# Kernel tuning notes

Hardware: AMD Instinct MI355X
Metric: run time of the kernel (lower is better)

## Reference

```python
import jax, jax.numpy as jnp
import numpy as np

NUM_ENT, NUM_REL, ES = 100000, 200, 128
B, N, K = 4, 1024, 50  # batch of tasks, triples per task, max one-hop neighbors


def setup_inputs() -> dict:
    key = jax.random.key(0)
    ks = jax.random.split(key, 10)
    return {
        "ent_emb": jax.random.normal(ks[0], (NUM_ENT, ES), jnp.float32),
        "rel_emb": jax.random.normal(ks[1], (NUM_REL, ES), jnp.float32),
        "W_bil": jax.random.normal(ks[2], (ES, ES), jnp.float32) * 0.05,
        "W1": jax.random.normal(ks[3], (ES, ES), jnp.float32) * 0.05,
        "b1": jax.random.normal(ks[4], (ES,), jnp.float32) * 0.05,
        "W2": jax.random.normal(ks[5], (ES, ES), jnp.float32) * 0.05,
        "b2": jax.random.normal(ks[6], (ES,), jnp.float32) * 0.05,
        "head_idx": jax.random.randint(ks[7], (B, N), 0, NUM_ENT, jnp.int64),
        "tail_idx": jax.random.randint(ks[8], (B, N), 0, NUM_ENT, jnp.int64),
        "conn_rel": jax.random.randint(ks[9], (NUM_ENT, K), 0, NUM_REL, jnp.int64),
    }


def reference(ent_emb, rel_emb, W_bil, W1, b1, W2, b2, head_idx, tail_idx, conn_rel):
    # Gather head/tail entity embeddings: [B, N, es]
    h_e = ent_emb[head_idx]
    t_e = ent_emb[tail_idx]
    weak_rel = t_e - h_e  # weak relation signal, [B, N, es]

    # Gather one-hop relation embeddings of head/tail neighborhoods: [B, N, K, es]
    h_rel = rel_emb[conn_rel[head_idx]]
    t_rel = rel_emb[conn_rel[tail_idx]]

    # Bilinear score (out_features=1, no bias): score = x1 @ W @ x2
    ws = jnp.einsum('ij,bnj->bni', W_bil, weak_rel)       # [B, N, es]
    h_att = jax.nn.softmax(jnp.einsum('bnki,bni->bnk', h_rel, ws), axis=-1)
    t_att = jax.nn.softmax(jnp.einsum('bnki,bni->bnk', t_rel, ws), axis=-1)

    # Attention-weighted aggregate over neighbors: [B, N, es]
    head = jnp.einsum('bnk,bnki->bni', h_att, h_rel)
    tail = jnp.einsum('bnk,bnki->bni', t_att, t_rel)

    # Fused linear + relu (torch Linear: x @ W.T + b)
    h = jax.nn.relu(head @ W1.T + b1 + h_e @ W2.T + b2)
    t = jax.nn.relu(tail @ W1.T + b1 + t_e @ W2.T + b2)

    # cat along the singleton dim=2 -> [B, N, 2, es]
    return jnp.stack((h, t), axis=2)
```

## Files before the change

kernel.cpp:

```cpp
#include <hip/hip_runtime.h>

#define ES 128
#define KN 50

__global__ __launch_bounds__(256) void prep_transpose(
    const float* __restrict__ Wb, const float* __restrict__ W1,
    const float* __restrict__ W2, float* __restrict__ wt)
{
    int n = blockIdx.x * 256 + threadIdx.x;
    int m = n >> 14;
    int r = (n >> 7) & 127;
    int c = n & 127;
    const float* src = (m == 0) ? Wb : ((m == 1) ? W1 : W2);
    wt[n] = src[c * ES + r];
}

#define LOADC(BUF, C) do {                                                   \
    _Pragma("unroll") for (int u = 0; u < 10; ++u) {                         \
        int k = (C) * 10 + u;                                                \
        int cid = (k < 32) ? cidA : cidB;                                    \
        int row = __shfl(cid, hb + (k & 31));                                \
        BUF[u] = *(const float4*)(rel + (size_t)row * ES + 4 * q);           \
    } } while (0)

#define REDUCE(BUF, C) do {                                                  \
    float pv[10];                                                            \
    _Pragma("unroll") for (int u = 0; u < 10; ++u)                           \
        pv[u] = BUF[u].x*ws4.x + BUF[u].y*ws4.y + BUF[u].z*ws4.z + BUF[u].w*ws4.w;\
    _Pragma("unroll") for (int s = 1; s < 32; s <<= 1)                       \
        { _Pragma("unroll") for (int u = 0; u < 10; ++u)                     \
            pv[u] += __shfl_xor(pv[u], s); }                                 \
    _Pragma("unroll") for (int u = 0; u < 10; ++u) {                         \
        int k = (C) * 10 + u;                                                \
        if (k < 32) s1 = (q == k)      ? pv[u] : s1;                         \
        else        s2 = (q == k - 32) ? pv[u] : s2;                         \
    } } while (0)

#define XADD(a) do { a.x += __shfl_xor(a.x, 32); a.y += __shfl_xor(a.y, 32); \
                     a.z += __shfl_xor(a.z, 32); a.w += __shfl_xor(a.w, 32); } while (0)

__global__ __launch_bounds__(64) void onehop_main(
    const float* __restrict__ ent, const float* __restrict__ rel,
    const float* __restrict__ b1, const float* __restrict__ b2,
    const int* __restrict__ hidx, const int* __restrict__ tidx,
    const int* __restrict__ conn,
    const float* __restrict__ WbT, const float* __restrict__ WT2,
    float* __restrict__ out, int npair, int num_ent, int num_rel)
{
    __shared__ float coef[4][2 * ES];
    __shared__ float wrbuf[2][ES];

    const int lane = threadIdx.x;
    const int q    = lane & 31;
    const int hi   = lane >> 5;
    const int hb   = lane & 32;
    const int pair0 = blockIdx.x * 2;
    const int pairB = min(pair0 + 1, npair - 1);

    int hid0 = min(max(hidx[pair0], 0), num_ent - 1);
    int tdi0 = min(max(tidx[pair0], 0), num_ent - 1);
    int hid1 = min(max(hidx[pairB], 0), num_ent - 1);
    int tdi1 = min(max(tidx[pairB], 0), num_ent - 1);

    float4 he0 = *(const float4*)(ent + (size_t)hid0 * ES + 4 * q);
    float4 te0 = *(const float4*)(ent + (size_t)tdi0 * ES + 4 * q);
    float4 he1 = *(const float4*)(ent + (size_t)hid1 * ES + 4 * q);
    float4 te1 = *(const float4*)(ent + (size_t)tdi1 * ES + 4 * q);

    const int cl = min(lane, KN - 1);
    int ch0 = min(max(conn[(size_t)hid0 * KN + cl], 0), num_rel - 1);
    int ct0 = min(max(conn[(size_t)tdi0 * KN + cl], 0), num_rel - 1);
    int ch1 = min(max(conn[(size_t)hid1 * KN + cl], 0), num_rel - 1);
    int ct1 = min(max(conn[(size_t)tdi1 * KN + cl], 0), num_rel - 1);

    #pragma unroll
    for (int p = 0; p < 2; ++p) {
        float4 he = p ? he1 : he0, te = p ? te1 : te0;
        int    ch = p ? ch1 : ch0, ct = p ? ct1 : ct0;

        float4 wr;
        wr.x = te.x - he.x; wr.y = te.y - he.y;
        wr.z = te.z - he.z; wr.w = te.w - he.w;
        *(float4*)(&wrbuf[p][4 * q]) = wr;
        *(float4*)(&coef[2 * p + hi][ES + 4 * q]) = hi ? te : he;

        int ctq  = __shfl(ct, q);
        int cidA = hi ? ctq : ch;
        int cB_l = __shfl(ch, q + 32);
        int cB_h = __shfl(ct, q + 32);
        int cidB = hi ? cB_h : cB_l;

        float4 ws4 = {0.f, 0.f, 0.f, 0.f};
        #pragma unroll 8
        for (int j = 0; j < ES; ++j) {
            float  wj = wrbuf[p][j];
            float4 wv = *(const float4*)(WbT + (size_t)j * ES + 4 * q);
            ws4.x += wj * wv.x; ws4.y += wj * wv.y;
            ws4.z += wj * wv.z; ws4.w += wj * wv.w;
        }

        float s1 = -1e30f, s2 = -1e30f;
        {
            float4 bufA[10], bufB[10];
            LOADC(bufA, 0); LOADC(bufB, 1);
            REDUCE(bufA, 0); LOADC(bufA, 2);
            REDUCE(bufB, 1); LOADC(bufB, 3);
            REDUCE(bufA, 2); LOADC(bufA, 4);
            REDUCE(bufB, 3);
            REDUCE(bufA, 4);
        }

        float m = fmaxf(s1, s2);
        #pragma unroll
        for (int s = 1; s < 32; s <<= 1) m = fmaxf(m, __shfl_xor(m, s));
        float e1 = __expf(s1 - m), e2 = __expf(s2 - m);
        float l = e1 + e2;
        #pragma unroll
        for (int s = 1; s < 32; s <<= 1) l += __shfl_xor(l, s);
        float rinv = 1.f / l;
        e1 *= rinv; e2 *= rinv;

        float4 agg = {0.f, 0.f, 0.f, 0.f};
        #pragma unroll 10
        for (int k = 0; k < KN; ++k) {
            int src = hb + (k & 31);
            float ev = __shfl((k < 32) ? e1 : e2, src);
            int row  = __shfl((k < 32) ? cidA : cidB, src);
            float4 v = *(const float4*)(rel + (size_t)row * ES + 4 * q);
            agg.x += ev * v.x; agg.y += ev * v.y;
            agg.z += ev * v.z; agg.w += ev * v.w;
        }
        *(float4*)(&coef[2 * p + hi][4 * q]) = agg;
    }

    float4 a0 = {0,0,0,0}, a1 = {0,0,0,0}, a2 = {0,0,0,0}, a3 = {0,0,0,0};
    #pragma unroll 4
    for (int j = 0; j < 2 * ES; j += 2) {
        float4 w = *(const float4*)(WT2 + (size_t)j * ES + 4 * lane);
        int jl = j + hi;
        float c0 = coef[0][jl], c1 = coef[1][jl];
        float c2 = coef[2][jl], c3 = coef[3][jl];
        a0.x += c0*w.x; a0.y += c0*w.y; a0.z += c0*w.z; a0.w += c0*w.w;
        a1.x += c1*w.x; a1.y += c1*w.y; a1.z += c1*w.z; a1.w += c1*w.w;
        a2.x += c2*w.x; a2.y += c2*w.y; a2.z += c2*w.z; a2.w += c2*w.w;
        a3.x += c3*w.x; a3.y += c3*w.y; a3.z += c3*w.z; a3.w += c3*w.w;
    }
    XADD(a0); XADD(a1); XADD(a2); XADD(a3);

    float4 bv1 = *(const float4*)(b1 + 4 * q);
    float4 bv2 = *(const float4*)(b2 + 4 * q);
    float4 bb;
    bb.x = bv1.x + bv2.x; bb.y = bv1.y + bv2.y;
    bb.z = bv1.z + bv2.z; bb.w = bv1.w + bv2.w;

    float4 oh, ot, o;
    oh.x = fmaxf(a0.x + bb.x, 0.f); oh.y = fmaxf(a0.y + bb.y, 0.f);
    oh.z = fmaxf(a0.z + bb.z, 0.f); oh.w = fmaxf(a0.w + bb.w, 0.f);
    ot.x = fmaxf(a1.x + bb.x, 0.f); ot.y = fmaxf(a1.y + bb.y, 0.f);
    ot.z = fmaxf(a1.z + bb.z, 0.f); ot.w = fmaxf(a1.w + bb.w, 0.f);
    o = hi ? ot : oh;
    *(float4*)(out + (size_t)(pair0 * 2 + hi) * ES + 4 * q) = o;

    if (pair0 + 1 < npair) {
        oh.x = fmaxf(a2.x + bb.x, 0.f); oh.y = fmaxf(a2.y + bb.y, 0.f);
        oh.z = fmaxf(a2.z + bb.z, 0.f); oh.w = fmaxf(a2.w + bb.w, 0.f);
        ot.x = fmaxf(a3.x + bb.x, 0.f); ot.y = fmaxf(a3.y + bb.y, 0.f);
        ot.z = fmaxf(a3.z + bb.z, 0.f); ot.w = fmaxf(a3.w + bb.w, 0.f);
        o = hi ? ot : oh;
        *(float4*)(out + (size_t)((pair0 + 1) * 2 + hi) * ES + 4 * q) = o;
    }
}

extern "C" void kernel_launch(void* const* d_in, const int* in_sizes, int n_in,
                              void* d_out, int out_size, void* d_ws, size_t ws_size,
                              hipStream_t stream) {
    const float* ent = (const float*)d_in[0];
    const float* rel = (const float*)d_in[1];
    const float* Wb  = (const float*)d_in[2];
    const float* W1  = (const float*)d_in[3];
    const float* b1  = (const float*)d_in[4];
    const float* W2  = (const float*)d_in[5];
    const float* b2  = (const float*)d_in[6];
    const int* hidx  = (const int*)d_in[7];
    const int* tidx  = (const int*)d_in[8];
    const int* conn  = (const int*)d_in[9];
    float* out = (float*)d_out;

    const int npair   = in_sizes[7];
    const int num_ent = in_sizes[0] / ES;
    const int num_rel = in_sizes[1] / ES;

    float* wt = (float*)d_ws;
    prep_transpose<<<192, 256, 0, stream>>>(Wb, W1, W2, wt);

    const int nblocks = (npair + 1) / 2;
    onehop_main<<<nblocks, 64, 0, stream>>>(
        ent, rel, b1, b2, hidx, tidx, conn,
        wt, wt + 16384, out, npair, num_ent, num_rel);
}
```

Before: 159.4 us.

## Precompute rel@Wbil table, use bf16 output weights, split pairs across two waves

The bilinear transform is moved onto the small relation table: each score becomes the dot product of weak_rel with a precomputed rel_emb@W_bil row. This removes the per-pair 128x128 matvec. The fused output GEMV now reads W1/W2 as bf16 converted by a prep kernel, halving weight traffic at some accuracy cost. Each block now runs two waves, one pair per wave. The output GEMV is split by K halves across the waves and the partials are combined through shared memory with barriers.

```diff
diff --git a/kernel.cpp b/kernel.cpp
--- a/kernel.cpp
+++ b/kernel.cpp
@@ -3,16 +3,35 @@
 #define ES 128
 #define KN 50
 
-__global__ __launch_bounds__(256) void prep_transpose(
-    const float* __restrict__ Wb, const float* __restrict__ W1,
-    const float* __restrict__ W2, float* __restrict__ wt)
+__device__ __forceinline__ unsigned short f32_to_bf16_rne(float f) {
+    unsigned u = __float_as_uint(f);
+    unsigned r = u + 0x7FFF + ((u >> 16) & 1);
+    return (unsigned short)(r >> 16);
+}
+__device__ __forceinline__ float bf16_to_f32(unsigned short u) {
+    return __uint_as_float(((unsigned)u) << 16);
+}
+
+__global__ __launch_bounds__(128) void prep_rwb(
+    const float* __restrict__ rel, const float* __restrict__ Wb,
+    float* __restrict__ rwb)
+{
+    const int r = blockIdx.x, j = threadIdx.x;
+    float acc = 0.f;
+    #pragma unroll 8
+    for (int i = 0; i < ES; ++i)
+        acc += rel[r * ES + i] * Wb[i * ES + j];
+    rwb[r * ES + j] = acc;
+}
+
+__global__ __launch_bounds__(256) void prep_wtbf(
+    const float* __restrict__ W1, const float* __restrict__ W2,
+    unsigned short* __restrict__ wtb)
 {
     int n = blockIdx.x * 256 + threadIdx.x;
-    int m = n >> 14;
-    int r = (n >> 7) & 127;
-    int c = n & 127;
-    const float* src = (m == 0) ? Wb : ((m == 1) ? W1 : W2);
-    wt[n] = src[c * ES + r];
+    int j = n >> 7, c = n & 127;
+    const float* src = (j < ES) ? W1 : W2;
+    wtb[n] = f32_to_bf16_rne(src[c * ES + (j & 127)]);
 }
 
 #define LOADC(BUF, C) do {                                                   \
@@ -20,13 +39,13 @@
         int k = (C) * 10 + u;                                                \
         int cid = (k < 32) ? cidA : cidB;                                    \
         int row = __shfl(cid, hb + (k & 31));                                \
-        BUF[u] = *(const float4*)(rel + (size_t)row * ES + 4 * q);           \
+        BUF[u] = *(const float4*)(RWb + (size_t)row * ES + 4 * q);           \
     } } while (0)
 
 #define REDUCE(BUF, C) do {                                                  \
     float pv[10];                                                            \
     _Pragma("unroll") for (int u = 0; u < 10; ++u)                           \
-        pv[u] = BUF[u].x*ws4.x + BUF[u].y*ws4.y + BUF[u].z*ws4.z + BUF[u].w*ws4.w;\
+        pv[u] = BUF[u].x*wr.x + BUF[u].y*wr.y + BUF[u].z*wr.z + BUF[u].w*wr.w;\
     _Pragma("unroll") for (int s = 1; s < 32; s <<= 1)                       \
         { _Pragma("unroll") for (int u = 0; u < 10; ++u)                     \
             pv[u] += __shfl_xor(pv[u], s); }                                 \
@@ -39,136 +58,117 @@
 #define XADD(a) do { a.x += __shfl_xor(a.x, 32); a.y += __shfl_xor(a.y, 32); \
                      a.z += __shfl_xor(a.z, 32); a.w += __shfl_xor(a.w, 32); } while (0)
 
-__global__ __launch_bounds__(64) void onehop_main(
+__global__ __launch_bounds__(128, 4) void onehop_main(
     const float* __restrict__ ent, const float* __restrict__ rel,
     const float* __restrict__ b1, const float* __restrict__ b2,
     const int* __restrict__ hidx, const int* __restrict__ tidx,
     const int* __restrict__ conn,
-    const float* __restrict__ WbT, const float* __restrict__ WT2,
+    const float* __restrict__ RWb, const unsigned short* __restrict__ WTB,
     float* __restrict__ out, int npair, int num_ent, int num_rel)
 {
     __shared__ float coef[4][2 * ES];
-    __shared__ float wrbuf[2][ES];
-
-    const int lane = threadIdx.x;
+    __shared__ float part[2][4][ES];
+
+    const int tid  = threadIdx.x;
+    const int wave = tid >> 6;
+    const int lane = tid & 63;
     const int q    = lane & 31;
     const int hi   = lane >> 5;
     const int hb   = lane & 32;
-    const int pair0 = blockIdx.x * 2;
-    const int pairB = min(pair0 + 1, npair - 1);
-
-    int hid0 = min(max(hidx[pair0], 0), num_ent - 1);
-    int tdi0 = min(max(tidx[pair0], 0), num_ent - 1);
-    int hid1 = min(max(hidx[pairB], 0), num_ent - 1);
-    int tdi1 = min(max(tidx[pairB], 0), num_ent - 1);
-
-    float4 he0 = *(const float4*)(ent + (size_t)hid0 * ES + 4 * q);
-    float4 te0 = *(const float4*)(ent + (size_t)tdi0 * ES + 4 * q);
-    float4 he1 = *(const float4*)(ent + (size_t)hid1 * ES + 4 * q);
-    float4 te1 = *(const float4*)(ent + (size_t)tdi1 * ES + 4 * q);
+
+    const int pair = min(blockIdx.x * 2 + wave, npair - 1);
+
+    int hid = min(max(hidx[pair], 0), num_ent - 1);
+    int tdi = min(max(tidx[pair], 0), num_ent - 1);
+
+    float4 he = *(const float4*)(ent + (size_t)hid * ES + 4 * q);
+    float4 te = *(const float4*)(ent + (size_t)tdi * ES + 4 * q);
+    float4 wr;
+    wr.x = te.x - he.x; wr.y = te.y - he.y;
+    wr.z = te.z - he.z; wr.w = te.w - he.w;
+    *(float4*)(&coef[2 * wave + hi][ES + 4 * q]) = hi ? te : he;
 
     const int cl = min(lane, KN - 1);
-    int ch0 = min(max(conn[(size_t)hid0 * KN + cl], 0), num_rel - 1);
-    int ct0 = min(max(conn[(size_t)tdi0 * KN + cl], 0), num_rel - 1);
-    int ch1 = min(max(conn[(size_t)hid1 * KN + cl], 0), num_rel - 1);
-    int ct1 = min(max(conn[(size_t)tdi1 * KN + cl], 0), num_rel - 1);
-
+    int ch = min(max(conn[(size_t)hid * KN + cl], 0), num_rel - 1);
+    int ct = min(max(conn[(size_t)tdi * KN + cl], 0), num_rel - 1);
+    int ctq  = __shfl(ct, q);
+    int cidA = hi ? ctq : ch;
+    int cB_l = __shfl(ch, q + 32);
+    int cB_h = __shfl(ct, q + 32);
+    int cidB = hi ? cB_h : cB_l;
+
+    float s1 = -1e30f, s2 = -1e30f;
+    {
+        float4 bufA[10], bufB[10];
+        LOADC(bufA, 0); LOADC(bufB, 1);
+        REDUCE(bufA, 0); LOADC(bufA, 2);
+        REDUCE(bufB, 1); LOADC(bufB, 3);
+        REDUCE(bufA, 2); LOADC(bufA, 4);
+        REDUCE(bufB, 3);
+        REDUCE(bufA, 4);
+    }
+
+    float m = fmaxf(s1, s2);
     #pragma unroll
-    for (int p = 0; p < 2; ++p) {
-        float4 he = p ? he1 : he0, te = p ? te1 : te0;
-        int    ch = p ? ch1 : ch0, ct = p ? ct1 : ct0;
-
-        float4 wr;
-        wr.x = te.x - he.x; wr.y = te.y - he.y;
-        wr.z = te.z - he.z; wr.w = te.w - he.w;
-        *(float4*)(&wrbuf[p][4 * q]) = wr;
-        *(float4*)(&coef[2 * p + hi][ES + 4 * q]) = hi ? te : he;
-
-        int ctq  = __shfl(ct, q);
-        int cidA = hi ? ctq : ch;
-        int cB_l = __shfl(ch, q + 32);
-        int cB_h = __shfl(ct, q + 32);
-        int cidB = hi ? cB_h : cB_l;
-
-        float4 ws4 = {0.f, 0.f, 0.f, 0.f};
-        #pragma unroll 8
-        for (int j = 0; j < ES; ++j) {
-            float  wj = wrbuf[p][j];
-            float4 wv = *(const float4*)(WbT + (size_t)j * ES + 4 * q);
-            ws4.x += wj * wv.x; ws4.y += wj * wv.y;
-            ws4.z += wj * wv.z; ws4.w += wj * wv.w;
-        }
-
-        float s1 = -1e30f, s2 = -1e30f;
-        {
-            float4 bufA[10], bufB[10];
-            LOADC(bufA, 0); LOADC(bufB, 1);
-            REDUCE(bufA, 0); LOADC(bufA, 2);
-            REDUCE(bufB, 1); LOADC(bufB, 3);
-            REDUCE(bufA, 2); LOADC(bufA, 4);
-            REDUCE(bufB, 3);
-            REDUCE(bufA, 4);
-        }
-
-        float m = fmaxf(s1, s2);
-        #pragma unroll
-        for (int s = 1; s < 32; s <<= 1) m = fmaxf(m, __shfl_xor(m, s));
-        float e1 = __expf(s1 - m), e2 = __expf(s2 - m);
-        float l = e1 + e2;
-        #pragma unroll
-        for (int s = 1; s < 32; s <<= 1) l += __shfl_xor(l, s);
-        float rinv = 1.f / l;
-        e1 *= rinv; e2 *= rinv;
-
-        float4 agg = {0.f, 0.f, 0.f, 0.f};
-        #pragma unroll 10
-        for (int k = 0; k < KN; ++k) {
-            int src = hb + (k & 31);
-            float ev = __shfl((k < 32) ? e1 : e2, src);
-            int row  = __shfl((k < 32) ? cidA : cidB, src);
-            float4 v = *(const float4*)(rel + (size_t)row * ES + 4 * q);
-            agg.x += ev * v.x; agg.y += ev * v.y;
-            agg.z += ev * v.z; agg.w += ev * v.w;
-        }
-        *(float4*)(&coef[2 * p + hi][4 * q]) = agg;
-    }
-
+    for (int s = 1; s < 32; s <<= 1) m = fmaxf(m, __shfl_xor(m, s));
+    float e1 = __expf(s1 - m), e2 = __expf(s2 - m);
+    float l = e1 + e2;
+    #pragma unroll
+    for (int s = 1; s < 32; s <<= 1) l += __shfl_xor(l, s);
+    float rinv = 1.f / l;
+    e1 *= rinv; e2 *= rinv;
+
+    float4 agg = {0.f, 0.f, 0.f, 0.f};
+    #pragma unroll 10
+    for (int k = 0; k < KN; ++k) {
+        int src = hb + (k & 31);
+        float ev = __shfl((k < 32) ? e1 : e2, src);
+        int row  = __shfl((k < 32) ? cidA : cidB, src);
+        float4 v = *(const float4*)(rel + (size_t)row * ES + 4 * q);
+        agg.x += ev * v.x; agg.y += ev * v.y;
+        agg.z += ev * v.z; agg.w += ev * v.w;
+    }
+    *(float4*)(&coef[2 * wave + hi][4 * q]) = agg;
+    __syncthreads();
+
+    const int jbase = wave << 7;
     float4 a0 = {0,0,0,0}, a1 = {0,0,0,0}, a2 = {0,0,0,0}, a3 = {0,0,0,0};
-    #pragma unroll 4
-    for (int j = 0; j < 2 * ES; j += 2) {
-        float4 w = *(const float4*)(WT2 + (size_t)j * ES + 4 * lane);
-        int jl = j + hi;
+    #pragma unroll 8
+    for (int jj = 0; jj < 64; ++jj) {
+        int j0 = jbase + 2 * jj;
+        ushort4 wv = *(const ushort4*)(WTB + (size_t)j0 * ES + 4 * lane);
+        float w0 = bf16_to_f32(wv.x), w1 = bf16_to_f32(wv.y);
+        float w2 = bf16_to_f32(wv.z), w3 = bf16_to_f32(wv.w);
+        int jl = j0 + hi;
         float c0 = coef[0][jl], c1 = coef[1][jl];
         float c2 = coef[2][jl], c3 = coef[3][jl];
-        a0.x += c0*w.x; a0.y += c0*w.y; a0.z += c0*w.z; a0.w += c0*w.w;
-        a1.x += c1*w.x; a1.y += c1*w.y; a1.z += c1*w.z; a1.w += c1*w.w;
-        a2.x += c2*w.x; a2.y += c2*w.y; a2.z += c2*w.z; a2.w += c2*w.w;
-        a3.x += c3*w.x; a3.y += c3*w.y; a3.z += c3*w.z; a3.w += c3*w.w;
+        a0.x += c0*w0; a0.y += c0*w1; a0.z += c0*w2; a0.w += c0*w3;
+        a1.x += c1*w0; a1.y += c1*w1; a1.z += c1*w2; a1.w += c1*w3;
+        a2.x += c2*w0; a2.y += c2*w1; a2.z += c2*w2; a2.w += c2*w3;
+        a3.x += c3*w0; a3.y += c3*w1; a3.z += c3*w2; a3.w += c3*w3;
     }
     XADD(a0); XADD(a1); XADD(a2); XADD(a3);
-
-    float4 bv1 = *(const float4*)(b1 + 4 * q);
-    float4 bv2 = *(const float4*)(b2 + 4 * q);
-    float4 bb;
-    bb.x = bv1.x + bv2.x; bb.y = bv1.y + bv2.y;
-    bb.z = bv1.z + bv2.z; bb.w = bv1.w + bv2.w;
-
-    float4 oh, ot, o;
-    oh.x = fmaxf(a0.x + bb.x, 0.f); oh.y = fmaxf(a0.y + bb.y, 0.f);
-    oh.z = fmaxf(a0.z + bb.z, 0.f); oh.w = fmaxf(a0.w + bb.w, 0.f);
-    ot.x = fmaxf(a1.x + bb.x, 0.f); ot.y = fmaxf(a1.y + bb.y, 0.f);
-    ot.z = fmaxf(a1.z + bb.z, 0.f); ot.w = fmaxf(a1.w + bb.w, 0.f);
-    o = hi ? ot : oh;
-    *(float4*)(out + (size_t)(pair0 * 2 + hi) * ES + 4 * q) = o;
-
-    if (pair0 + 1 < npair) {
-        oh.x = fmaxf(a2.x + bb.x, 0.f); oh.y = fmaxf(a2.y + bb.y, 0.f);
-        oh.z = fmaxf(a2.z + bb.z, 0.f); oh.w = fmaxf(a2.w + bb.w, 0.f);
-        ot.x = fmaxf(a3.x + bb.x, 0.f); ot.y = fmaxf(a3.y + bb.y, 0.f);
-        ot.z = fmaxf(a3.z + bb.z, 0.f); ot.w = fmaxf(a3.w + bb.w, 0.f);
-        o = hi ? ot : oh;
-        *(float4*)(out + (size_t)((pair0 + 1) * 2 + hi) * ES + 4 * q) = o;
-    }
+    if (!hi) {
+        *(float4*)(&part[wave][0][4 * q]) = a0;
+        *(float4*)(&part[wave][1][4 * q]) = a1;
+        *(float4*)(&part[wave][2][4 * q]) = a2;
+        *(float4*)(&part[wave][3][4 * q]) = a3;
+    }
+    __syncthreads();
+
+    const int o = tid >> 5, q2 = tid & 31;
+    float4 p0 = *(const float4*)(&part[0][o][4 * q2]);
+    float4 p1 = *(const float4*)(&part[1][o][4 * q2]);
+    float4 v1 = *(const float4*)(b1 + 4 * q2);
+    float4 v2 = *(const float4*)(b2 + 4 * q2);
+    float4 r;
+    r.x = fmaxf(p0.x + p1.x + v1.x + v2.x, 0.f);
+    r.y = fmaxf(p0.y + p1.y + v1.y + v2.y, 0.f);
+    r.z = fmaxf(p0.z + p1.z + v1.z + v2.z, 0.f);
+    r.w = fmaxf(p0.w + p1.w + v1.w + v2.w, 0.f);
+    const int orow = blockIdx.x * 4 + o;
+    if (orow < 2 * npair)
+        *(float4*)(out + (size_t)orow * ES + 4 * q2) = r;
 }
 
 extern "C" void kernel_launch(void* const* d_in, const int* in_sizes, int n_in,
@@ -190,11 +190,14 @@
     const int num_ent = in_sizes[0] / ES;
     const int num_rel = in_sizes[1] / ES;
 
-    float* wt = (float*)d_ws;
-    prep_transpose<<<192, 256, 0, stream>>>(Wb, W1, W2, wt);
+    float* rwb = (float*)d_ws;
+    unsigned short* wtb = (unsigned short*)(rwb + (size_t)num_rel * ES);
+
+    prep_rwb<<<num_rel, 128, 0, stream>>>(rel, Wb, rwb);
+    prep_wtbf<<<(2 * ES * ES) / 256, 256, 0, stream>>>(W1, W2, wtb);
 
     const int nblocks = (npair + 1) / 2;
-    onehop_main<<<nblocks, 64, 0, stream>>>(
+    onehop_main<<<nblocks, 128, 0, stream>>>(
         ent, rel, b1, b2, hidx, tidx, conn,
-        wt, wt + 16384, out, npair, num_ent, num_rel);
-}
+        rwb, wtb, out, npair, num_ent, num_rel);
+}
```

Result: faster. 146.7 us (-8.0%).
